# Performance work log

Hardware: AMD Instinct MI355X
Metric: run time of the kernel (lower is better)

## Reference

```python
import jax, jax.numpy as jnp
import numpy as np

B, T, D, H = 2, 2048, 1024, 16
DH = D // H

def setup_inputs() -> dict:
    key = jax.random.key(0)
    ks = jax.random.split(key, 5)
    s = 1.0 / np.sqrt(D)
    return {
        "x": jax.random.normal(ks[0], (B, T, D), dtype=jnp.float32),
        "w_q": jax.random.normal(ks[1], (D, D), dtype=jnp.float32) * s,
        "w_k": jax.random.normal(ks[2], (D, D), dtype=jnp.float32) * s,
        "w_v": jax.random.normal(ks[3], (D, D), dtype=jnp.float32) * s,
        "w_o": jax.random.normal(ks[4], (D, D), dtype=jnp.float32) * s,
    }

def reference(x, w_q, w_k, w_v, w_o):
    # Linear(bias=False): y = x @ W.T
    q = jnp.einsum('btd,ed->bte', x, w_q).reshape(B, T, H, DH).transpose(0, 2, 1, 3)
    k = jnp.einsum('btd,ed->bte', x, w_k).reshape(B, T, H, DH).transpose(0, 2, 1, 3)
    v = jnp.einsum('btd,ed->bte', x, w_v).reshape(B, T, H, DH).transpose(0, 2, 1, 3)
    scores = jnp.einsum('bhqd,bhkd->bhqk', q, k) / np.sqrt(DH)  # [B,H,T,T]
    causal = jnp.triu(jnp.ones((T, T), dtype=bool), k=1)
    scores = jnp.where(causal[None, None, :, :], -jnp.inf, scores)
    attn = jax.nn.softmax(scores, axis=-1)
    ctx = jnp.einsum('bhqk,bhkd->bhqd', attn, v)
    ctx = ctx.transpose(0, 2, 1, 3).reshape(B, T, D)
    out = jnp.einsum('btd,ed->bte', ctx, w_o)
    return out
```

## Files before the change

kernel.cpp:

```cpp
#include <hip/hip_runtime.h>
#include <hip/hip_bf16.h>

typedef __bf16 bf16_t;
typedef __attribute__((ext_vector_type(8))) __bf16 bf16x8;
typedef __attribute__((ext_vector_type(4))) __bf16 bf16x4;
typedef __attribute__((ext_vector_type(4))) float f32x4;
typedef __attribute__((ext_vector_type(16))) float f32x16;
typedef __attribute__((ext_vector_type(2))) int i32x2;

#define B_ 2
#define T_ 2048
#define D_ 1024
#define H_ 16
#define DH_ 64
#define RS_ 3072

static __device__ __forceinline__ f32x4 mfma16(bf16x8 a, bf16x8 b, f32x4 c) {
  return __builtin_amdgcn_mfma_f32_16x16x32_bf16(a, b, c, 0, 0, 0);
}
static __device__ __forceinline__ f32x16 mfma32(bf16x8 a, bf16x8 b, f32x16 c) {
  return __builtin_amdgcn_mfma_f32_32x32x16_bf16(a, b, c, 0, 0, 0);
}
static __device__ __forceinline__ void gld16(const bf16_t* g, bf16_t* l) {
  __builtin_amdgcn_global_load_lds(
      (const __attribute__((address_space(1))) unsigned int*)g,
      (__attribute__((address_space(3))) unsigned int*)l, 16, 0, 0);
}
static __device__ __forceinline__ unsigned lds_addr(const bf16_t* p) {
  return (unsigned)(uintptr_t)(const __attribute__((address_space(3))) bf16_t*)p;
}
static __device__ __forceinline__ i32x2 tr64(unsigned a) {
  i32x2 d;
  asm volatile("ds_read_b64_tr_b16 %0, %1" : "=v"(d) : "v"(a));
  return d;
}
static __device__ __forceinline__ i32x2 tr64o(unsigned a) {
  i32x2 d;
  asm volatile("ds_read_b64_tr_b16 %0, %1 offset:128" : "=v"(d) : "v"(a));
  return d;
}
static __device__ __forceinline__ unsigned pk2(float lo, float hi2) {
  unsigned short a = __builtin_bit_cast(unsigned short, (bf16_t)lo);
  unsigned short b = __builtin_bit_cast(unsigned short, (bf16_t)hi2);
  return (unsigned)a | ((unsigned)b << 16);
}

#define WAITV4 { asm volatile("s_waitcnt vmcnt(4)" ::: "memory"); __builtin_amdgcn_sched_barrier(0); }
#define WAITV0 { asm volatile("s_waitcnt vmcnt(0)" ::: "memory"); __builtin_amdgcn_sched_barrier(0); }
#define BAR    { __builtin_amdgcn_s_barrier(); __builtin_amdgcn_sched_barrier(0); }

__global__ __launch_bounds__(256) void cvt_x(const float* __restrict__ in,
                                             bf16_t* __restrict__ out, int n4) {
  int i = blockIdx.x * 256 + threadIdx.x;
  if (i >= n4) return;
  float4 f = reinterpret_cast<const float4*>(in)[i];
  bf16x4 o;
  o[0] = (bf16_t)f.x; o[1] = (bf16_t)f.y; o[2] = (bf16_t)f.z; o[3] = (bf16_t)f.w;
  reinterpret_cast<bf16x4*>(out)[i] = o;
}

__global__ __launch_bounds__(256) void cvt_w4(const float* __restrict__ w0,
                                              const float* __restrict__ w1,
                                              const float* __restrict__ w2,
                                              const float* __restrict__ w3,
                                              bf16_t* __restrict__ out, int n4each) {
  const float* in = blockIdx.y == 0 ? w0 : blockIdx.y == 1 ? w1 : blockIdx.y == 2 ? w2 : w3;
  bf16_t* o = out + (size_t)blockIdx.y * (size_t)n4each * 4;
  int i = blockIdx.x * 256 + threadIdx.x;
  if (i >= n4each) return;
  float4 f = reinterpret_cast<const float4*>(in)[i];
  bf16x4 v;
  v[0] = (bf16_t)f.x; v[1] = (bf16_t)f.y; v[2] = (bf16_t)f.z; v[3] = (bf16_t)f.w;
  reinterpret_cast<bf16x4*>(o)[i] = v;
}

template <bool STORE_F32, bool QSCALE>
__global__ __launch_bounds__(256) void gemm_nt(const bf16_t* __restrict__ A,
                                               const bf16_t* __restrict__ Bm,
                                               void* __restrict__ Cv,
                                               int M, int N, int K) {
  __shared__ __align__(16) bf16_t As[128 * 64];
  __shared__ __align__(16) bf16_t Bs[128 * 64];
  const int tid = threadIdx.x, lane = tid & 63, wave = tid >> 6;
  const int brow = blockIdx.y * 128, bcol = blockIdx.x * 128;
  const int row0 = (wave >> 1) * 64, col0 = (wave & 1) * 64;
  const int lrow = lane >> 3, lcol = (lane & 7) * 8;
  const float cscale = (QSCALE && bcol < 1024) ? 0.18033688011112042f : 1.0f;

  f32x4 acc[4][4];
#pragma unroll
  for (int m = 0; m < 4; ++m)
#pragma unroll
    for (int n = 0; n < 4; ++n) acc[m][n] = f32x4{0.f, 0.f, 0.f, 0.f};

  for (int k0 = 0; k0 < K; k0 += 64) {
    const bf16_t* ga = A + (size_t)(brow + 32 * wave + lrow) * K + k0 + lcol;
    const bf16_t* gb = Bm + (size_t)(bcol + 32 * wave + lrow) * K + k0 + lcol;
#pragma unroll
    for (int s = 0; s < 4; ++s) {
      gld16(ga + (size_t)(8 * s) * K, &As[(32 * wave + 8 * s) * 64]);
      gld16(gb + (size_t)(8 * s) * K, &Bs[(32 * wave + 8 * s) * 64]);
    }
    __syncthreads();
#pragma unroll
    for (int kk = 0; kk < 2; ++kk) {
      const int ko = kk * 32 + (lane >> 4) * 8;
      bf16x8 af[4], bfr[4];
#pragma unroll
      for (int m = 0; m < 4; ++m)
        af[m] = *(const bf16x8*)&As[(row0 + 16 * m + (lane & 15)) * 64 + ko];
#pragma unroll
      for (int n = 0; n < 4; ++n)
        bfr[n] = *(const bf16x8*)&Bs[(col0 + 16 * n + (lane & 15)) * 64 + ko];
#pragma unroll
      for (int m = 0; m < 4; ++m)
#pragma unroll
        for (int n = 0; n < 4; ++n) acc[m][n] = mfma16(af[m], bfr[n], acc[m][n]);
    }
    __syncthreads();
  }
  const int crow = brow + row0 + (lane >> 4) * 4;
  const int ccol = bcol + col0 + (lane & 15);
#pragma unroll
  for (int m = 0; m < 4; ++m)
#pragma unroll
    for (int n = 0; n < 4; ++n)
#pragma unroll
      for (int r = 0; r < 4; ++r) {
        size_t idx = (size_t)(crow + 16 * m + r) * N + (ccol + 16 * n);
        float v = acc[m][n][r] * cscale;
        if (STORE_F32) reinterpret_cast<float*>(Cv)[idx] = v;
        else reinterpret_cast<bf16_t*>(Cv)[idx] = (bf16_t)v;
      }
}

#define CROW(r) ((((r) & 3) + 8 * ((r) >> 2)) + 4 * hi)

__global__ __launch_bounds__(256, 1) void attn_fwd(const bf16_t* __restrict__ qkv,
                                                   bf16_t* __restrict__ ctx) {
  __shared__ __align__(128) bf16_t KV[3][2][64 * 64];
  const int tid = threadIdx.x;
  const int lane = tid & 63;
  const int wv = tid >> 6;
  const int bh = blockIdx.x, p = blockIdx.y;
  const int b = bh >> 4, h = bh & 15;
  const bf16_t* Qg = qkv + (size_t)b * T_ * RS_ + h * DH_;
  const bf16_t* Kg = Qg + 1024;
  const bf16_t* Vg = Qg + 2048;
  bf16_t* Cg = ctx + (size_t)b * T_ * D_ + h * DH_;

  const int hi = lane >> 5;
  const int l31 = lane & 31;
  const int l15 = lane & 15;

  auto stage = [&](int bi, int kt) {
    bf16_t* Kb = &KV[bi][0][0];
    bf16_t* Vb = &KV[bi][1][0];
#pragma unroll
    for (int i = 0; i < 2; ++i) {
      int c2 = i * 256 + tid;
      int r = c2 >> 3, g8 = (c2 & 7) ^ (r & 7);
      gld16(Kg + (size_t)(kt * 64 + r) * RS_ + g8 * 8, Kb + i * 2048 + wv * 512);
    }
#pragma unroll
    for (int i = 0; i < 2; ++i) {
      int c2 = i * 256 + tid;
      int pn = c2 >> 7, k = (c2 >> 1) & 63, half = c2 & 1;
      gld16(Vg + (size_t)(kt * 64 + k) * RS_ + pn * 16 + half * 8, Vb + i * 2048 + wv * 512);
    }
  };

#pragma unroll 1
  for (int phase = 0; phase < 2; ++phase) {
    const int c = phase ? (63 - 4 * p - wv) : (4 * p + wv);
    const int q0 = c * 32;
    const int mynkt = (c >> 1) + 1;
    const int maxnkt = phase ? (32 - 2 * p) : (2 * p + 2);

    BAR;
    stage(0, 0);
    stage(1, 1);

    bf16x8 qf[4];
#pragma unroll
    for (int d = 0; d < 4; ++d)
      qf[d] = *(const bf16x8*)&Qg[(size_t)(q0 + l31) * RS_ + d * 16 + hi * 8];

    f32x16 o[2];
#pragma unroll
    for (int n = 0; n < 2; ++n)
#pragma unroll
      for (int r = 0; r < 16; ++r) o[n][r] = 0.f;
    float mrow = -1e30f, lsum = 0.f;

#pragma unroll 1
    for (int kt = 0; kt < maxnkt; ++kt) {
      if (kt + 1 < maxnkt) { WAITV4 } else { WAITV0 }
      BAR;
      if (kt + 2 < maxnkt) stage((kt + 2) % 3, kt + 2);

      if (kt < mynkt) {
        const bf16_t* Kb = &KV[kt % 3][0][0];
        bf16x8 kf[2][4];
#pragma unroll
        for (int t = 0; t < 2; ++t)
#pragma unroll
          for (int d = 0; d < 4; ++d) {
            int row = 32 * t + l31;
            int col = ((d * 2 + hi) ^ (row & 7)) * 8;
            kf[t][d] = *(const bf16x8*)&Kb[row * 64 + col];
          }
        bf16x8 vf[2][4];
        {
          unsigned vb = lds_addr(&KV[kt % 3][1][0]);
#pragma unroll
          for (int n2 = 0; n2 < 2; ++n2)
#pragma unroll
            for (int ks = 0; ks < 4; ++ks) {
              int pn = 2 * n2 + (l31 >> 4);
              int k0 = ks * 16 + hi * 8;
              unsigned a = vb + pn * 2048 + k0 * 32 + l15 * 8;
              i32x2 lo = tr64(a);
              i32x2 hi4 = tr64o(a);
              union { unsigned u[4]; bf16x8 v; } uu;
              uu.u[0] = (unsigned)lo[0]; uu.u[1] = (unsigned)lo[1];
              uu.u[2] = (unsigned)hi4[0]; uu.u[3] = (unsigned)hi4[1];
              vf[n2][ks] = uu.v;
            }
        }
        asm volatile("s_waitcnt lgkmcnt(0)" ::: "memory");
        __builtin_amdgcn_sched_barrier(0);

        f32x16 st[2];
#pragma unroll
        for (int t = 0; t < 2; ++t) {
#pragma unroll
          for (int r = 0; r < 16; ++r) st[t][r] = 0.f;
#pragma unroll
          for (int d = 0; d < 4; ++d) st[t] = mfma32(kf[t][d], qf[d], st[t]);
        }
        if (kt == mynkt - 1) {
#pragma unroll
          for (int t = 0; t < 2; ++t)
#pragma unroll
            for (int r = 0; r < 16; ++r)
              if (kt * 64 + 32 * t + CROW(r) > q0 + l31) st[t][r] = -1e30f;
        }
        float pm = -1e30f;
#pragma unroll
        for (int t = 0; t < 2; ++t)
#pragma unroll
          for (int r = 0; r < 16; ++r) pm = fmaxf(pm, st[t][r]);
        pm = fmaxf(pm, __shfl_xor(pm, 32));
        if (!__all(pm - mrow <= 11.0f)) {
          float mn = fmaxf(mrow, pm);
          float scl = exp2f(mrow - mn);
          mrow = mn;
          lsum *= scl;
#pragma unroll
          for (int r = 0; r < 16; ++r) {
            float sr = __shfl(scl, CROW(r));
            o[0][r] *= sr;
            o[1][r] *= sr;
          }
        }
        float ps = 0.f;
#pragma unroll
        for (int t = 0; t < 2; ++t)
#pragma unroll
          for (int r = 0; r < 16; ++r) {
            float e = exp2f(st[t][r] - mrow);
            st[t][r] = e;
            ps += e;
          }
        ps += __shfl_xor(ps, 32);
        lsum += ps;
        unsigned pk[2][8];
#pragma unroll
        for (int t = 0; t < 2; ++t)
#pragma unroll
          for (int j = 0; j < 8; ++j) pk[t][j] = pk2(st[t][2 * j], st[t][2 * j + 1]);
#pragma unroll
        for (int ks = 0; ks < 4; ++ks) {
          const int t = ks >> 1, rb = (ks & 1) * 4;
          unsigned s0 = hi ? pk[t][rb] : pk[t][rb + 2];
          unsigned s1 = hi ? pk[t][rb + 1] : pk[t][rb + 3];
          unsigned r0 = (unsigned)__shfl_xor((int)s0, 32);
          unsigned r1 = (unsigned)__shfl_xor((int)s1, 32);
          union { unsigned u[4]; bf16x8 v; } w;
          if (hi == 0) {
            w.u[0] = pk[t][rb]; w.u[1] = pk[t][rb + 1]; w.u[2] = r0; w.u[3] = r1;
          } else {
            w.u[0] = r0; w.u[1] = r1; w.u[2] = pk[t][rb + 2]; w.u[3] = pk[t][rb + 3];
          }
          o[0] = mfma32(w.v, vf[0][ks], o[0]);
          o[1] = mfma32(w.v, vf[1][ks], o[1]);
        }
      }
    }

#pragma unroll
    for (int r = 0; r < 16; ++r) {
      float li = __shfl(lsum, CROW(r));
      float inv = 1.0f / li;
      int qrow = q0 + CROW(r);
#pragma unroll
      for (int n2 = 0; n2 < 2; ++n2)
        Cg[(size_t)qrow * D_ + n2 * 32 + l31] = (bf16_t)(o[n2][r] * inv);
    }
  }
}

extern "C" void kernel_launch(void* const* d_in, const int* in_sizes, int n_in,
                              void* d_out, int out_size, void* d_ws, size_t ws_size,
                              hipStream_t stream) {
  const float* x   = (const float*)d_in[0];
  const float* w_q = (const float*)d_in[1];
  const float* w_k = (const float*)d_in[2];
  const float* w_v = (const float*)d_in[3];
  const float* w_o = (const float*)d_in[4];

  const int M = B_ * T_;
  const size_t XN = (size_t)M * D_;
  const size_t WN = (size_t)D_ * D_;

  bf16_t* ws = (bf16_t*)d_ws;
  bf16_t* xb   = ws;
  bf16_t* wqb  = xb + XN;
  bf16_t* wob  = wqb + 3 * WN;
  bf16_t* qkv  = wob + WN;
  bf16_t* ctx  = qkv + (size_t)M * RS_;

  cvt_x<<<(int)(XN / 4 / 256), 256, 0, stream>>>(x, xb, (int)(XN / 4));
  cvt_w4<<<dim3((int)(WN / 4 / 256), 4), 256, 0, stream>>>(w_q, w_k, w_v, w_o, wqb, (int)(WN / 4));

  gemm_nt<false, true><<<dim3(RS_ / 128, M / 128), 256, 0, stream>>>(xb, wqb, qkv, M, RS_, D_);

  attn_fwd<<<dim3(B_ * H_, 8), 256, 0, stream>>>(qkv, ctx);

  gemm_nt<true, false><<<dim3(D_ / 128, M / 128), 256, 0, stream>>>(ctx, wob, d_out, M, D_, D_);
}
```

Measured before the change: 156.1 us.

## Triple-buffer GEMM LDS tiles with async prefetch two k-steps ahead

New measurement: 138.9 us. 1.12x faster.

```diff
diff --git a/kernel.cpp b/kernel.cpp
--- a/kernel.cpp
+++ b/kernel.cpp
@@ -48,6 +48,7 @@
 #define WAITV4 { asm volatile("s_waitcnt vmcnt(4)" ::: "memory"); __builtin_amdgcn_sched_barrier(0); }
 #define WAITV0 { asm volatile("s_waitcnt vmcnt(0)" ::: "memory"); __builtin_amdgcn_sched_barrier(0); }
 #define BAR    { __builtin_amdgcn_s_barrier(); __builtin_amdgcn_sched_barrier(0); }
+#define WAITL0 { asm volatile("s_waitcnt lgkmcnt(0)" ::: "memory"); __builtin_amdgcn_sched_barrier(0); }
 
 __global__ __launch_bounds__(256) void cvt_x(const float* __restrict__ in,
                                              bf16_t* __restrict__ out, int n4) {
@@ -79,12 +80,12 @@
                                                const bf16_t* __restrict__ Bm,
                                                void* __restrict__ Cv,
                                                int M, int N, int K) {
-  __shared__ __align__(16) bf16_t As[128 * 64];
-  __shared__ __align__(16) bf16_t Bs[128 * 64];
+  __shared__ __align__(16) bf16_t As[3][128 * 32];
+  __shared__ __align__(16) bf16_t Bs[3][128 * 32];
   const int tid = threadIdx.x, lane = tid & 63, wave = tid >> 6;
+  const int l15 = lane & 15;
   const int brow = blockIdx.y * 128, bcol = blockIdx.x * 128;
   const int row0 = (wave >> 1) * 64, col0 = (wave & 1) * 64;
-  const int lrow = lane >> 3, lcol = (lane & 7) * 8;
   const float cscale = (QSCALE && bcol < 1024) ? 0.18033688011112042f : 1.0f;
 
   f32x4 acc[4][4];
@@ -93,34 +94,49 @@
 #pragma unroll
     for (int n = 0; n < 4; ++n) acc[m][n] = f32x4{0.f, 0.f, 0.f, 0.f};
 
-  for (int k0 = 0; k0 < K; k0 += 64) {
-    const bf16_t* ga = A + (size_t)(brow + 32 * wave + lrow) * K + k0 + lcol;
-    const bf16_t* gb = Bm + (size_t)(bcol + 32 * wave + lrow) * K + k0 + lcol;
-#pragma unroll
-    for (int s = 0; s < 4; ++s) {
-      gld16(ga + (size_t)(8 * s) * K, &As[(32 * wave + 8 * s) * 64]);
-      gld16(gb + (size_t)(8 * s) * K, &Bs[(32 * wave + 8 * s) * 64]);
-    }
-    __syncthreads();
-#pragma unroll
-    for (int kk = 0; kk < 2; ++kk) {
-      const int ko = kk * 32 + (lane >> 4) * 8;
-      bf16x8 af[4], bfr[4];
-#pragma unroll
-      for (int m = 0; m < 4; ++m)
-        af[m] = *(const bf16x8*)&As[(row0 + 16 * m + (lane & 15)) * 64 + ko];
-#pragma unroll
-      for (int n = 0; n < 4; ++n)
-        bfr[n] = *(const bf16x8*)&Bs[(col0 + 16 * n + (lane & 15)) * 64 + ko];
-#pragma unroll
-      for (int m = 0; m < 4; ++m)
-#pragma unroll
-        for (int n = 0; n < 4; ++n) acc[m][n] = mfma16(af[m], bfr[n], acc[m][n]);
-    }
-    __syncthreads();
+  const int nst = K >> 5;
+  const int srow = tid >> 2;
+  const int sc8 = (tid & 3) * 8;
+  auto stage = [&](int bi, int ks) {
+    const int k0 = ks * 32;
+#pragma unroll
+    for (int i = 0; i < 2; ++i)
+      gld16(A + (size_t)(brow + 64 * i + srow) * K + k0 + sc8,
+            &As[bi][2048 * i + 512 * wave]);
+#pragma unroll
+    for (int i = 0; i < 2; ++i)
+      gld16(Bm + (size_t)(bcol + 64 * i + srow) * K + k0 + sc8,
+            &Bs[bi][2048 * i + 512 * wave]);
+  };
+
+  stage(0, 0);
+  stage(1, 1);
+
+#pragma unroll 1
+  for (int ks = 0; ks < nst; ++ks) {
+    if (ks + 1 < nst) { WAITV4 } else { WAITV0 }
+    BAR;
+    if (ks + 2 < nst) stage((ks + 2) % 3, ks + 2);
+
+    const bf16_t* Ab = &As[ks % 3][0];
+    const bf16_t* Bb = &Bs[ks % 3][0];
+    const int ko = (lane >> 4) * 8;
+    bf16x8 af[4], bfr[4];
+#pragma unroll
+    for (int m = 0; m < 4; ++m)
+      af[m] = *(const bf16x8*)&Ab[(row0 + 16 * m + l15) * 32 + ko];
+#pragma unroll
+    for (int n = 0; n < 4; ++n)
+      bfr[n] = *(const bf16x8*)&Bb[(col0 + 16 * n + l15) * 32 + ko];
+    WAITL0;
+#pragma unroll
+    for (int m = 0; m < 4; ++m)
+#pragma unroll
+      for (int n = 0; n < 4; ++n) acc[m][n] = mfma16(af[m], bfr[n], acc[m][n]);
   }
+
   const int crow = brow + row0 + (lane >> 4) * 4;
-  const int ccol = bcol + col0 + (lane & 15);
+  const int ccol = bcol + col0 + l15;
 #pragma unroll
   for (int m = 0; m < 4; ++m)
 #pragma unroll
@@ -228,8 +244,7 @@
               vf[n2][ks] = uu.v;
             }
         }
-        asm volatile("s_waitcnt lgkmcnt(0)" ::: "memory");
-        __builtin_amdgcn_sched_barrier(0);
+        WAITL0;
 
         f32x16 st[2];
 #pragma unroll
```
